# Optimization experiments

Measured on AMD Instinct MI355X. Metric: run time of the kernel, lower is better.

The kernel has to match this reference:

```python
import jax, jax.numpy as jnp
import numpy as np

B, S, D, H = 4, 2048, 1024, 16
HD = D // H
SCALE = HD ** -0.5


def setup_inputs() -> dict:
    key = jax.random.key(0)
    ks = jax.random.split(key, 5)
    std = D ** -0.5
    return {
        "x": jax.random.normal(ks[0], (B, S, D), jnp.float32),
        "wq": jax.random.normal(ks[1], (D, D), jnp.float32) * std,
        "bq": jnp.zeros((D,), jnp.float32),
        "wk": jax.random.normal(ks[2], (D, D), jnp.float32) * std,
        "bk": jnp.zeros((D,), jnp.float32),
        "wv": jax.random.normal(ks[3], (D, D), jnp.float32) * std,
        "bv": jnp.zeros((D,), jnp.float32),
        "wo": jax.random.normal(ks[4], (D, D), jnp.float32) * std,
        "bo": jnp.zeros((D,), jnp.float32),
    }


def reference(x, wq, bq, wk, bk, wv, bv, wo, bo):
    # projections; weights stored as [in, out] so y = x @ w + b
    q = (x @ wq + bq).reshape(B, S, H, HD).transpose(0, 2, 1, 3)  # [B,H,S,HD]
    k = (x @ wk + bk).reshape(B, S, H, HD).transpose(0, 2, 1, 3)
    v = (x @ wv + bv).reshape(B, S, H, HD).transpose(0, 2, 1, 3)
    attn = jnp.einsum("bhqd,bhkd->bhqk", q, k) * SCALE  # [B,H,S,S]
    attn = jax.nn.softmax(attn, axis=-1)
    out = jnp.einsum("bhqk,bhkd->bhqd", attn, v)  # [B,H,S,HD]
    out = out.transpose(0, 2, 1, 3).reshape(B, S, D)
    return out @ wo + bo
```

## Files before the change

### kernel.cpp

```cpp
#include <hip/hip_runtime.h>
#include <stdint.h>


typedef __attribute__((ext_vector_type(8))) short bf16x8;
typedef __attribute__((ext_vector_type(4))) short bf16x4;
typedef __attribute__((ext_vector_type(4))) float f32x4;
typedef __attribute__((ext_vector_type(16))) float f32x16;
typedef __attribute__((ext_vector_type(4))) int i32x4;
typedef unsigned short u16;
typedef unsigned int u32;

#define AS1 __attribute__((address_space(1)))
#define AS3 __attribute__((address_space(3)))

#define SCALE_L2E 0.18033688011112042f

__device__ __forceinline__ void gld_lds16(const void* g, void* l) {
  __builtin_amdgcn_global_load_lds((const AS1 void*)g, (AS3 void*)l, 16, 0, 0);
}

__device__ __forceinline__ u16 f2bf(float f) {
  u32 x = __builtin_bit_cast(u32, f);
  x += 0x7fff + ((x >> 16) & 1);
  return (u16)(x >> 16);
}

__device__ __forceinline__ u16 f2bf_fast(float a) {
#if __has_builtin(__builtin_amdgcn_cvt_pk_bf16_f32)
  auto v = __builtin_amdgcn_cvt_pk_bf16_f32(a, a);
  return (u16)(__builtin_bit_cast(u32, v) & 0xffffu);
#else
  return f2bf(a);
#endif
}

__device__ __forceinline__ u32 pk2(float a, float b) {
#if __has_builtin(__builtin_amdgcn_cvt_pk_bf16_f32)
  return __builtin_bit_cast(u32, __builtin_amdgcn_cvt_pk_bf16_f32(a, b));
#else
  return (u32)f2bf(a) | ((u32)f2bf(b) << 16);
#endif
}

__device__ __forceinline__ float exp2_fast(float x) {
#if __has_builtin(__builtin_amdgcn_exp2f)
  return __builtin_amdgcn_exp2f(x);
#else
  return exp2f(x);
#endif
}

__device__ __forceinline__ f32x16 zero16() {
  f32x16 z;
#pragma unroll
  for (int i = 0; i < 16; ++i) z[i] = 0.f;
  return z;
}

__global__ __launch_bounds__(256) void convert_x(const float* __restrict__ x,
                                                 u16* __restrict__ xb) {
  int i = (blockIdx.x * 256 + threadIdx.x) * 4;
  float4 v = *(const float4*)(x + i);
  ushort4 o;
  o.x = f2bf(v.x); o.y = f2bf(v.y); o.z = f2bf(v.z); o.w = f2bf(v.w);
  *(ushort4*)(xb + i) = o;
}

__global__ __launch_bounds__(256) void pack_weights(
    const float* __restrict__ wq, const float* __restrict__ wk,
    const float* __restrict__ wv, const float* __restrict__ wo,
    u16* __restrict__ wt_qkv, u16* __restrict__ wt_o) {
  __shared__ float tile[64][65];
  int mat = blockIdx.z;
  const float* src = (mat == 0) ? wq : (mat == 1) ? wk : (mat == 2) ? wv : wo;
  int k0 = blockIdx.y * 64, j0 = blockIdx.x * 64;
  int t = threadIdx.x;
  int lr = t >> 6;
  int lc = t & 63;
#pragma unroll
  for (int it = 0; it < 16; ++it) {
    int r = it * 4 + lr;
    tile[r][lc] = src[(size_t)(k0 + r) * 1024 + j0 + lc];
  }
  __syncthreads();
  u16* dst = (mat == 3) ? wt_o : (wt_qkv + (size_t)mat * 1024 * 1024);
#pragma unroll
  for (int it = 0; it < 16; ++it) {
    int nl = it * 4 + lr;
    float v = tile[lc][nl];
    if (mat == 0) v *= SCALE_L2E;
    dst[(size_t)(j0 + nl) * 1024 + k0 + lc] = f2bf(v);
  }
}

template <int MODE>
__global__ __launch_bounds__(256, 3) void gemm_bt(
    const u16* __restrict__ A, const u16* __restrict__ Bt,
    const float* __restrict__ bias0, const float* __restrict__ bias1,
    const float* __restrict__ bias2,
    void* __restrict__ out0v, void* __restrict__ out1v, void* __restrict__ out2v) {
  __shared__ u16 lA[128 * 32];
  __shared__ u16 lB[128 * 32];
  const int K = 1024;
  int tid = threadIdx.x;
  int wave = tid >> 6, lane = tid & 63;

  int bid = blockIdx.x;
  int m0, n0;
  if constexpr (MODE == 0) {
    int xcd = bid & 7, j = bid >> 3;
    n0 = (xcd * 3 + j % 3) * 128;
    m0 = (j / 3) * 128;
  } else {
    n0 = (bid & 7) * 128;
    m0 = (bid >> 3) * 128;
  }
  int wm = (wave & 1) * 64, wn = (wave >> 1) * 64;

  f32x4 acc[4][4];
#pragma unroll
  for (int i = 0; i < 4; ++i)
#pragma unroll
    for (int j = 0; j < 4; ++j) acc[i][j] = f32x4{0.f, 0.f, 0.f, 0.f};

  int srow = lane >> 2;
  int scol = (lane & 3) * 8;

  for (int k0 = 0; k0 < K; k0 += 32) {
#pragma unroll
    for (int c = 0; c < 2; ++c) {
      int rbase = wave * 32 + c * 16;
      gld_lds16(A + (size_t)(m0 + rbase + srow) * K + k0 + scol, lA + rbase * 32);
      gld_lds16(Bt + (size_t)(n0 + rbase + srow) * K + k0 + scol, lB + rbase * 32);
    }
    __syncthreads();
    bf16x8 af[4], bfr[4];
#pragma unroll
    for (int mt = 0; mt < 4; ++mt)
      af[mt] = *(const bf16x8*)(lA + (wm + mt * 16 + (lane & 15)) * 32 + (lane >> 4) * 8);
#pragma unroll
    for (int nt = 0; nt < 4; ++nt)
      bfr[nt] = *(const bf16x8*)(lB + (wn + nt * 16 + (lane & 15)) * 32 + (lane >> 4) * 8);
#pragma unroll
    for (int mt = 0; mt < 4; ++mt)
#pragma unroll
      for (int nt = 0; nt < 4; ++nt)
        acc[mt][nt] = __builtin_amdgcn_mfma_f32_16x16x32_bf16(af[mt], bfr[nt], acc[mt][nt], 0, 0, 0);
    __syncthreads();
  }

  int rbase0 = m0 + wm + (lane >> 4) * 4;
  int cbase = n0 + wn + (lane & 15);
#pragma unroll
  for (int nt = 0; nt < 4; ++nt) {
    int col = cbase + nt * 16;
    if constexpr (MODE == 0) {
      int mat = col >> 10, j = col & 1023;
      const float* bp = (mat == 0) ? bias0 : (mat == 1) ? bias1 : bias2;
      float bv = bp[j];
      if (mat == 0) bv *= SCALE_L2E;
      if (mat == 2) {
        int h = j >> 6, hd = j & 63;
        u16* base = (u16*)out2v;
#pragma unroll
        for (int mt = 0; mt < 4; ++mt) {
          int row0 = rbase0 + mt * 16;
          int b = row0 >> 11, s = row0 & 2047;
          int ci = s >> 6, sl = s & 63;
          int slice = sl >> 4, srem = sl & 15;
          size_t off = (size_t)(b * 16 + h) * 131072 + ci * 4096 + slice * 1024
                     + ((srem >> 2) & 1) * 512 + hd * 8 + (srem >> 3) * 4;
          ushort4 pk;
          pk.x = f2bf_fast(acc[mt][nt][0] + bv);
          pk.y = f2bf_fast(acc[mt][nt][1] + bv);
          pk.z = f2bf_fast(acc[mt][nt][2] + bv);
          pk.w = f2bf_fast(acc[mt][nt][3] + bv);
          *(ushort4*)(base + off) = pk;
        }
      } else {
        u16* base = (mat == 0) ? (u16*)out0v : (u16*)out1v;
#pragma unroll
        for (int mt = 0; mt < 4; ++mt)
#pragma unroll
          for (int r = 0; r < 4; ++r) {
            int row = rbase0 + mt * 16 + r;
            base[(size_t)row * 1024 + j] = f2bf_fast(acc[mt][nt][r] + bv);
          }
      }
    } else {
      float bv = bias0[col];
      float* o = (float*)out0v;
#pragma unroll
      for (int mt = 0; mt < 4; ++mt)
#pragma unroll
        for (int r = 0; r < 4; ++r) {
          int row = rbase0 + mt * 16 + r;
          o[(size_t)row * 1024 + col] = acc[mt][nt][r] + bv;
        }
    }
  }
}

__global__ __launch_bounds__(512, 2) void flash_attn(
    const u16* __restrict__ Q, const u16* __restrict__ Kb,
    const u16* __restrict__ Vg, u16* __restrict__ ctx) {
  __shared__ u16 lK[2][64 * 32];
  __shared__ u16 lV[4096];
  int tid = threadIdx.x, wave = tid >> 6, lane = tid & 63;

  int F = blockIdx.x;
  int xcd = F & 7, idx = F >> 3;
  int bh = xcd * 8 + (idx >> 2);
  int q0 = (idx & 3) * 512;
  int b = bh >> 4, h = bh & 15;
  const u16* Qp = Q + (size_t)b * 2048 * 1024 + h * 64;
  const u16* Kp = Kb + (size_t)b * 2048 * 1024 + h * 64;
  const u16* Vp = Vg + (size_t)bh * 131072;

  int ql = lane & 31;
  int hi = lane >> 5;

  bf16x8 qf[2][4];
#pragma unroll
  for (int qt = 0; qt < 2; ++qt) {
    const u16* qrow = Qp + (size_t)(q0 + wave * 64 + qt * 32 + ql) * 1024;
#pragma unroll
    for (int kk = 0; kk < 4; ++kk)
      qf[qt][kk] = *(const bf16x8*)(qrow + kk * 16 + hi * 8);
  }

  float lsum[2] = {0.f, 0.f};
  f32x16 o[2][2];
#pragma unroll
  for (int qt = 0; qt < 2; ++qt)
#pragma unroll
    for (int dh = 0; dh < 2; ++dh) o[qt][dh] = zero16();

  int srow = lane >> 2;
  int schunk = (((lane & 3) ^ ((lane >> 3) & 3)) * 8);
  int kk_w = wave & 1;
  int rb = wave >> 1;
  int stg_row = rb * 16 + srow;
  int rkey = ((lane & 15) >> 1) & 3;

  const u16* gK = Kp + (size_t)stg_row * 1024 + kk_w * 32 + schunk;
  const u16* gV = Vp + wave * 512 + lane * 8;
  u16* wK = lK[kk_w] + rb * 512 + lane * 8;
  u16* wV = lV + wave * 512 + lane * 8;

  i32x4 ldK = *(const i32x4*)gK;
  i32x4 ldV = *(const i32x4*)gV;
  *(i32x4*)wK = ldK;
  *(i32x4*)wV = ldV;
  __syncthreads();

  for (int s0 = 0; s0 < 2048; s0 += 64) {
    bool more = (s0 + 64 < 2048);
    if (more) {
      ldK = *(const i32x4*)(gK + (size_t)(s0 + 64) * 1024);
      ldV = *(const i32x4*)(gV + (size_t)(s0 + 64) * 64);
    }

#pragma unroll
    for (int sb = 0; sb < 2; ++sb) {
      bf16x8 kf[4];
      int krb = (sb * 32 + ql) * 32;
#pragma unroll
      for (int kk = 0; kk < 4; ++kk)
        kf[kk] = *(const bf16x8*)(lK[kk >> 1] + krb + ((((kk & 1) << 1) | hi) ^ rkey) * 8);

      f32x16 sa0 = zero16(), sa1 = zero16();
#pragma unroll
      for (int kk = 0; kk < 4; ++kk) {
        sa0 = __builtin_amdgcn_mfma_f32_32x32x16_bf16(kf[kk], qf[0][kk], sa0, 0, 0, 0);
        sa1 = __builtin_amdgcn_mfma_f32_32x32x16_bf16(kf[kk], qf[1][kk], sa1, 0, 0, 0);
      }

      bf16x8 pu[2][2];
#pragma unroll
      for (int qt = 0; qt < 2; ++qt) {
        float p[16];
#pragma unroll
        for (int r = 0; r < 16; ++r)
          p[r] = exp2_fast(qt == 0 ? sa0[r] : sa1[r]);
        float a0 = (p[0] + p[1]) + (p[2] + p[3]);
        float a1 = (p[4] + p[5]) + (p[6] + p[7]);
        float a2 = (p[8] + p[9]) + (p[10] + p[11]);
        float a3 = (p[12] + p[13]) + (p[14] + p[15]);
        lsum[qt] += (a0 + a1) + (a2 + a3);
#pragma unroll
        for (int ss = 0; ss < 2; ++ss) {
          union { u32 w[4]; bf16x8 v; } pk_;
          pk_.w[0] = pk2(p[8 * ss + 0], p[8 * ss + 1]);
          pk_.w[1] = pk2(p[8 * ss + 2], p[8 * ss + 3]);
          pk_.w[2] = pk2(p[8 * ss + 4], p[8 * ss + 5]);
          pk_.w[3] = pk2(p[8 * ss + 6], p[8 * ss + 7]);
          pu[qt][ss] = pk_.v;
        }
      }

#pragma unroll
      for (int ss = 0; ss < 2; ++ss) {
        int vbase = (sb * 2 + ss) * 1024 + hi * 512 + ql * 8;
#pragma unroll
        for (int dh = 0; dh < 2; ++dh) {
          bf16x8 vf = *(const bf16x8*)(lV + vbase + dh * 256);
          o[0][dh] = __builtin_amdgcn_mfma_f32_32x32x16_bf16(vf, pu[0][ss], o[0][dh], 0, 0, 0);
          o[1][dh] = __builtin_amdgcn_mfma_f32_32x32x16_bf16(vf, pu[1][ss], o[1][dh], 0, 0, 0);
        }
      }
    }

    __syncthreads();
    if (more) {
      *(i32x4*)wK = ldK;
      *(i32x4*)wV = ldV;
    }
    __syncthreads();
  }

#pragma unroll
  for (int qt = 0; qt < 2; ++qt) {
    float rs = lsum[qt] + __shfl_xor(lsum[qt], 32);
    float inv = 1.0f / fmaxf(rs, 1e-30f);
    int q = q0 + wave * 64 + qt * 32 + ql;
    size_t rowbase = ((size_t)(b * 2048 + q) * 16 + h) * 64;
#pragma unroll
    for (int dh = 0; dh < 2; ++dh)
#pragma unroll
      for (int rr = 0; rr < 4; ++rr) {
        ushort4 pk;
        pk.x = f2bf_fast(o[qt][dh][4 * rr + 0] * inv);
        pk.y = f2bf_fast(o[qt][dh][4 * rr + 1] * inv);
        pk.z = f2bf_fast(o[qt][dh][4 * rr + 2] * inv);
        pk.w = f2bf_fast(o[qt][dh][4 * rr + 3] * inv);
        *(ushort4*)(ctx + rowbase + dh * 32 + rr * 8 + hi * 4) = pk;
      }
  }
}

extern "C" void kernel_launch(void* const* d_in, const int* in_sizes, int n_in,
                              void* d_out, int out_size, void* d_ws, size_t ws_size,
                              hipStream_t stream) {
  const float* x  = (const float*)d_in[0];
  const float* wq = (const float*)d_in[1];
  const float* bq = (const float*)d_in[2];
  const float* wk = (const float*)d_in[3];
  const float* bk = (const float*)d_in[4];
  const float* wv = (const float*)d_in[5];
  const float* bv = (const float*)d_in[6];
  const float* wo = (const float*)d_in[7];
  const float* bo = (const float*)d_in[8];

  u16* ws = (u16*)d_ws;
  u16* xb     = ws;
  u16* wt_qkv = xb + (size_t)8192 * 1024;
  u16* wt_o   = wt_qkv + (size_t)3072 * 1024;
  u16* Qb     = wt_o + (size_t)1024 * 1024;
  u16* Kbuf   = Qb + (size_t)8192 * 1024;
  u16* Vgb    = Kbuf + (size_t)8192 * 1024;
  u16* ctx    = Vgb + (size_t)8192 * 1024;

  convert_x<<<8192, 256, 0, stream>>>(x, xb);
  pack_weights<<<dim3(16, 16, 4), 256, 0, stream>>>(wq, wk, wv, wo, wt_qkv, wt_o);
  gemm_bt<0><<<1536, 256, 0, stream>>>(xb, wt_qkv, bq, bk, bv, Qb, Kbuf, Vgb);
  flash_attn<<<256, 512, 0, stream>>>(Qb, Kbuf, Vgb, ctx);
  gemm_bt<1><<<512, 256, 0, stream>>>(ctx, wt_o, bo, nullptr, nullptr,
                                      d_out, nullptr, nullptr);
}
```

Before: 282.3 us.

## Replace QKV GEMM with 256x256-tile double-buffered kernel

The fused QKV projection now runs in a new kernel using 256x256 output tiles, 512 threads, a BK of 64 and double-buffered LDS, so the next K slice loads while the current one is multiplied. Larger tiles raise arithmetic intensity and cut global traffic per FLOP, and the prefetch hides load latency. The cost is 128KB of LDS per block and a large accumulator set, which limits occupancy, and only 384 blocks for the whole machine. The old MODE 0 path is removed from the generic GEMM.

After: 306.4 us. +8.5%, slower.

```diff
diff --git a/kernel.cpp b/kernel.cpp
--- a/kernel.cpp
+++ b/kernel.cpp
@@ -93,6 +93,114 @@
   }
 }
 
+__global__ __launch_bounds__(512, 2) void gemm256_qkv(
+    const u16* __restrict__ A, const u16* __restrict__ Bt,
+    const float* __restrict__ bias0, const float* __restrict__ bias1,
+    const float* __restrict__ bias2,
+    u16* __restrict__ outQ, u16* __restrict__ outK, u16* __restrict__ outV) {
+  __shared__ u16 lA[2][256 * 64];
+  __shared__ u16 lB[2][256 * 64];
+  int tid = threadIdx.x;
+  int wave = tid >> 6, lane = tid & 63;
+  int wr = wave >> 2, wc = wave & 3;
+
+  int bid = blockIdx.x;
+  int xcd = bid & 7, j = bid >> 3;
+  int m0 = (xcd * 4 + (j & 3)) * 256;
+  int n0 = (j >> 2) * 256;
+
+  f32x4 acc[8][4];
+#pragma unroll
+  for (int fm = 0; fm < 8; ++fm)
+#pragma unroll
+    for (int fn = 0; fn < 4; ++fn) acc[fm][fn] = f32x4{0.f, 0.f, 0.f, 0.f};
+
+  int srow = lane >> 3;
+  int scol = (lane & 7) * 8;
+  int fr = lane & 15;
+  int kq = (lane >> 4) * 8;
+
+#pragma unroll
+  for (int seg = 0; seg < 4; ++seg) {
+    int r0 = seg * 64 + wave * 8;
+    gld_lds16(A + (size_t)(m0 + r0 + srow) * 1024 + scol, &lA[0][r0 * 64]);
+    gld_lds16(Bt + (size_t)(n0 + r0 + srow) * 1024 + scol, &lB[0][r0 * 64]);
+  }
+  __syncthreads();
+
+  int cur = 0;
+  for (int kt = 0; kt < 16; ++kt) {
+    if (kt < 15) {
+      int k1 = (kt + 1) * 64;
+#pragma unroll
+      for (int seg = 0; seg < 4; ++seg) {
+        int r0 = seg * 64 + wave * 8;
+        gld_lds16(A + (size_t)(m0 + r0 + srow) * 1024 + k1 + scol,
+                  &lA[cur ^ 1][r0 * 64]);
+        gld_lds16(Bt + (size_t)(n0 + r0 + srow) * 1024 + k1 + scol,
+                  &lB[cur ^ 1][r0 * 64]);
+      }
+    }
+    const u16* la = lA[cur];
+    const u16* lb = lB[cur];
+#pragma unroll
+    for (int ks = 0; ks < 2; ++ks) {
+      bf16x8 af[8], bfv[4];
+#pragma unroll
+      for (int fm = 0; fm < 8; ++fm)
+        af[fm] = *(const bf16x8*)(la + (wr * 128 + fm * 16 + fr) * 64 + ks * 32 + kq);
+#pragma unroll
+      for (int fn = 0; fn < 4; ++fn)
+        bfv[fn] = *(const bf16x8*)(lb + (wc * 64 + fn * 16 + fr) * 64 + ks * 32 + kq);
+#pragma unroll
+      for (int fm = 0; fm < 8; ++fm)
+#pragma unroll
+        for (int fn = 0; fn < 4; ++fn)
+          acc[fm][fn] = __builtin_amdgcn_mfma_f32_16x16x32_bf16(
+              af[fm], bfv[fn], acc[fm][fn], 0, 0, 0);
+    }
+    __syncthreads();
+    cur ^= 1;
+  }
+
+  int mat = n0 >> 10;
+  const float* bp = (mat == 0) ? bias0 : (mat == 1) ? bias1 : bias2;
+  int rb0 = m0 + wr * 128 + (lane >> 4) * 4;
+  int jb = (n0 & 1023) + wc * 64;
+#pragma unroll
+  for (int fn = 0; fn < 4; ++fn) {
+    int jj = jb + fn * 16 + fr;
+    float bv = bp[jj];
+    if (mat == 0) bv *= SCALE_L2E;
+    if (mat == 2) {
+      int h = jj >> 6, hd = jj & 63;
+#pragma unroll
+      for (int fm = 0; fm < 8; ++fm) {
+        int row0 = rb0 + fm * 16;
+        int b = row0 >> 11, s = row0 & 2047;
+        int ci = s >> 6, sl = s & 63;
+        int slice = sl >> 4, srem = sl & 15;
+        size_t off = (size_t)(b * 16 + h) * 131072 + ci * 4096 + slice * 1024
+                   + ((srem >> 2) & 1) * 512 + hd * 8 + (srem >> 3) * 4;
+        ushort4 pk;
+        pk.x = f2bf_fast(acc[fm][fn][0] + bv);
+        pk.y = f2bf_fast(acc[fm][fn][1] + bv);
+        pk.z = f2bf_fast(acc[fm][fn][2] + bv);
+        pk.w = f2bf_fast(acc[fm][fn][3] + bv);
+        *(ushort4*)(outV + off) = pk;
+      }
+    } else {
+      u16* base = (mat == 0) ? outQ : outK;
+#pragma unroll
+      for (int fm = 0; fm < 8; ++fm)
+#pragma unroll
+        for (int rr = 0; rr < 4; ++rr)
+          base[(size_t)(rb0 + fm * 16 + rr) * 1024 + jj] =
+              f2bf_fast(acc[fm][fn][rr] + bv);
+    }
+  }
+}
+
 template <int MODE>
 __global__ __launch_bounds__(256, 3) void gemm_bt(
     const u16* __restrict__ A, const u16* __restrict__ Bt,
@@ -106,22 +214,15 @@
   int wave = tid >> 6, lane = tid & 63;
 
   int bid = blockIdx.x;
-  int m0, n0;
-  if constexpr (MODE == 0) {
-    int xcd = bid & 7, j = bid >> 3;
-    n0 = (xcd * 3 + j % 3) * 128;
-    m0 = (j / 3) * 128;
-  } else {
-    n0 = (bid & 7) * 128;
-    m0 = (bid >> 3) * 128;
-  }
+  int n0 = (bid & 7) * 128;
+  int m0 = (bid >> 3) * 128;
   int wm = (wave & 1) * 64, wn = (wave >> 1) * 64;
 
   f32x4 acc[4][4];
 #pragma unroll
   for (int i = 0; i < 4; ++i)
 #pragma unroll
-    for (int j = 0; j < 4; ++j) acc[i][j] = f32x4{0.f, 0.f, 0.f, 0.f};
+    for (int jj = 0; jj < 4; ++jj) acc[i][jj] = f32x4{0.f, 0.f, 0.f, 0.f};
 
   int srow = lane >> 2;
   int scol = (lane & 3) * 8;
@@ -154,50 +255,15 @@
 #pragma unroll
   for (int nt = 0; nt < 4; ++nt) {
     int col = cbase + nt * 16;
-    if constexpr (MODE == 0) {
-      int mat = col >> 10, j = col & 1023;
-      const float* bp = (mat == 0) ? bias0 : (mat == 1) ? bias1 : bias2;
-      float bv = bp[j];
-      if (mat == 0) bv *= SCALE_L2E;
-      if (mat == 2) {
-        int h = j >> 6, hd = j & 63;
-        u16* base = (u16*)out2v;
-#pragma unroll
-        for (int mt = 0; mt < 4; ++mt) {
-          int row0 = rbase0 + mt * 16;
-          int b = row0 >> 11, s = row0 & 2047;
-          int ci = s >> 6, sl = s & 63;
-          int slice = sl >> 4, srem = sl & 15;
-          size_t off = (size_t)(b * 16 + h) * 131072 + ci * 4096 + slice * 1024
-                     + ((srem >> 2) & 1) * 512 + hd * 8 + (srem >> 3) * 4;
-          ushort4 pk;
-          pk.x = f2bf_fast(acc[mt][nt][0] + bv);
-          pk.y = f2bf_fast(acc[mt][nt][1] + bv);
-          pk.z = f2bf_fast(acc[mt][nt][2] + bv);
-          pk.w = f2bf_fast(acc[mt][nt][3] + bv);
-          *(ushort4*)(base + off) = pk;
-        }
-      } else {
-        u16* base = (mat == 0) ? (u16*)out0v : (u16*)out1v;
-#pragma unroll
-        for (int mt = 0; mt < 4; ++mt)
-#pragma unroll
-          for (int r = 0; r < 4; ++r) {
-            int row = rbase0 + mt * 16 + r;
-            base[(size_t)row * 1024 + j] = f2bf_fast(acc[mt][nt][r] + bv);
-          }
-      }
-    } else {
-      float bv = bias0[col];
-      float* o = (float*)out0v;
-#pragma unroll
-      for (int mt = 0; mt < 4; ++mt)
-#pragma unroll
-        for (int r = 0; r < 4; ++r) {
-          int row = rbase0 + mt * 16 + r;
-          o[(size_t)row * 1024 + col] = acc[mt][nt][r] + bv;
-        }
-    }
+    float bv = bias0[col];
+    float* o = (float*)out0v;
+#pragma unroll
+    for (int mt = 0; mt < 4; ++mt)
+#pragma unroll
+      for (int r = 0; r < 4; ++r) {
+        int row = rbase0 + mt * 16 + r;
+        o[(size_t)row * 1024 + col] = acc[mt][nt][r] + bv;
+      }
   }
 }
 
@@ -363,7 +429,7 @@
 
   convert_x<<<8192, 256, 0, stream>>>(x, xb);
   pack_weights<<<dim3(16, 16, 4), 256, 0, stream>>>(wq, wk, wv, wo, wt_qkv, wt_o);
-  gemm_bt<0><<<1536, 256, 0, stream>>>(xb, wt_qkv, bq, bk, bv, Qb, Kbuf, Vgb);
+  gemm256_qkv<<<384, 512, 0, stream>>>(xb, wt_qkv, bq, bk, bv, Qb, Kbuf, Vgb);
   flash_attn<<<256, 512, 0, stream>>>(Qb, Kbuf, Vgb, ctx);
   gemm_bt<1><<<512, 256, 0, stream>>>(ctx, wt_o, bo, nullptr, nullptr,
                                       d_out, nullptr, nullptr);
```
